# Kernel tuning notes

Hardware: AMD Instinct MI355X
Metric: run time of the kernel (lower is better)

The kernel has to match this reference:

```python
import jax, jax.numpy as jnp
import numpy as np

D_MODEL = 512
D_EMB = 300
D_FIXED = 30000
D_EXT = 32000
BS, L, J, N, T = 8, 256, 48, 32, 48


def setup_inputs() -> dict:
    key = jax.random.key(0)
    ks = jax.random.split(key, 32)
    s = 0.02
    def nrm(k, shape, scale=0.02):
        return jax.random.normal(k, shape, dtype=jnp.float32) * scale
    inp = {
        "Mp": jax.random.normal(ks[0], (BS, L, D_MODEL), dtype=jnp.float32),
        "Mq": jax.random.normal(ks[1], (BS, J, D_MODEL), dtype=jnp.float32),
        "Mqa": jax.random.normal(ks[2], (BS, N, D_MODEL), dtype=jnp.float32),
        "Mnlg": jax.random.normal(ks[3], (BS, T, D_MODEL), dtype=jnp.float32),
        "mask_p": jnp.ones((BS, L, 1), dtype=bool),
        "mask_q": jnp.ones((BS, J, 1), dtype=bool),
        "mask_qa": jnp.ones((BS, N, 1), dtype=bool),
        "source_ext": jax.random.randint(ks[4], (BS, L + J + N), 0, D_EXT, dtype=jnp.int64) if jax.config.jax_enable_x64 else jax.random.randint(ks[4], (BS, L + J + N), 0, D_EXT).astype(jnp.int32),
        "special_mask": jnp.ones((D_FIXED,), dtype=bool).at[jnp.array([0, 1, 2, 3])].set(False),
        "d_ext_vocab": D_EXT,
    }
    # additive attention params for question / qa / passage branches
    names = ["q", "a", "p"]
    for i, nme in enumerate(names):
        base = 5 + 5 * i
        inp[f"Wk_{nme}"] = nrm(ks[base + 0], (D_MODEL, D_MODEL))
        inp[f"bk_{nme}"] = jnp.zeros((D_MODEL,), dtype=jnp.float32)
        inp[f"Wq_{nme}"] = nrm(ks[base + 1], (D_MODEL, D_MODEL))
        inp[f"bq_{nme}"] = jnp.zeros((D_MODEL,), dtype=jnp.float32)
        inp[f"v_{nme}"] = nrm(ks[base + 2], (D_MODEL,))
    # vocab generator: Linear(d_model, d_emb) -> Linear(d_emb, d_fixed, bias=False)
    inp["W1"] = nrm(ks[20], (D_MODEL, D_EMB))
    inp["b1"] = jnp.zeros((D_EMB,), dtype=jnp.float32)
    inp["W2"] = nrm(ks[21], (D_EMB, D_FIXED))
    # mixture: Linear(4*d_model, 4) + softmax
    inp["Wm"] = nrm(ks[22], (4 * D_MODEL, 4))
    inp["bm"] = jnp.zeros((4,), dtype=jnp.float32)
    return inp


def _additive_attn(K, V, Q, mask, Wk, bk, Wq, bq, v):
    # K,V: [b,S,d]; Q: [b,T,d]; mask: [b,S,1] bool
    Kp = K @ Wk + bk                                  # [b,S,d]
    Qp = Q @ Wq + bq                                  # [b,T,d]
    scores = jnp.einsum("btsd,d->bts", jnp.tanh(Qp[:, :, None, :] + Kp[:, None, :, :]), v)
    scores = jnp.where(mask[:, None, :, 0], scores, -1e9)
    attn = jax.nn.softmax(scores, axis=-1)            # [b,T,S]
    ctx = jnp.einsum("bts,bsd->btd", attn, V)         # [b,T,d]
    return ctx, attn


def reference(Mp, Mq, Mqa, Mnlg, mask_p, mask_q, mask_qa, source_ext, special_mask,
              Wk_q, bk_q, Wq_q, bq_q, v_q,
              Wk_a, bk_a, Wq_a, bq_a, v_a,
              Wk_p, bk_p, Wq_p, bq_p, v_p,
              W1, b1, W2, Wm, bm, d_ext_vocab):
    d_fixed = special_mask.shape[0]
    bs, Tq, _ = Mnlg.shape

    ctx_q, q_distr = _additive_attn(Mq, Mq, Mnlg, mask_q, Wk_q, bk_q, Wq_q, bq_q, v_q)
    ctx_a, qa_distr = _additive_attn(Mqa, Mqa, Mnlg, mask_qa, Wk_a, bk_a, Wq_a, bq_a, v_a)
    ctx_p, p_distr = _additive_attn(Mp, Mp, Mnlg, mask_p, Wk_p, bk_p, Wq_p, bq_p, v_p)

    # fixed-vocab distribution with special tokens masked out
    logits = (Mnlg @ W1 + b1) @ W2                    # [b,T,d_fixed]
    logits = jnp.where(special_mask[None, None, :], logits, -1e9)
    fixed_vocab_distr = jax.nn.softmax(logits, axis=-1)

    # mixture weights
    mix_in = jnp.concatenate([Mnlg, ctx_q, ctx_a, ctx_p], axis=-1)  # [b,T,4d]
    lambdas = jax.nn.softmax(mix_in @ Wm + bm, axis=-1)             # [b,T,4]
    lam_v, lam_q, lam_qa, lam_p = jnp.split(lambdas, 4, axis=-1)

    fixed_vocab_distr = fixed_vocab_distr * lam_v
    source_distr = jnp.concatenate([p_distr * lam_p, q_distr * lam_q, qa_distr * lam_qa], axis=-1)  # [b,T,S_tot]

    # scatter-add over extended vocab (math-equivalent to one_hot + matmul)
    def _scatter(src, idx):
        # src: [T,S_tot], idx: [S_tot]
        return jnp.zeros((Tq, d_ext_vocab), src.dtype).at[:, idx].add(src)

    ext_vocab_distr = jax.vmap(_scatter)(source_distr, source_ext)  # [b,T,d_ext]
    ext_vocab_distr = ext_vocab_distr.at[:, :, :d_fixed].add(fixed_vocab_distr)
    return ext_vocab_distr, lambdas
```

## Files before the change

kernel.cpp:

```cpp
#include <hip/hip_runtime.h>
#include <math.h>

#define BS     8
#define LL     256
#define JJ     48
#define NN     32
#define TT     48
#define DM     512
#define DEMB   300
#define DFIX   30000
#define DEXT   32000
#define SRC_TOT (LL + JJ + NN)
#define ROWS   (BS * TT)
#define NT     235
#define KH     320

typedef float f32x4  __attribute__((ext_vector_type(4)));
typedef short bf16x8 __attribute__((ext_vector_type(8)));

__device__ __forceinline__ short f2bf(float f) {
    union { float f; unsigned u; } v; v.f = f;
    return (short)((v.u + 0x7FFFu + ((v.u >> 16) & 1u)) >> 16);
}
__device__ __forceinline__ float bf2f(short s) {
    union { unsigned u; float f; } v;
    v.u = ((unsigned)(unsigned short)s) << 16;
    return v.f;
}
__device__ __forceinline__ float fast_exp2(float x) {
#if __has_builtin(__builtin_amdgcn_exp2f)
    return __builtin_amdgcn_exp2f(x);
#else
    return exp2f(x);
#endif
}
__device__ __forceinline__ float fast_rcp(float x) {
#if __has_builtin(__builtin_amdgcn_rcpf)
    return __builtin_amdgcn_rcpf(x);
#else
    return 1.f / x;
#endif
}
__device__ __forceinline__ float fast_tanh(float x) {
    x = fminf(fmaxf(x, -15.f), 15.f);
    const float e = fast_exp2(x * 2.885390082f);
    return (e - 1.f) * fast_rcp(e + 1.f);
}
__device__ __forceinline__ bool smask_true(const void* smask, bool byteLayout, int i)
{
    if (byteLayout) return ((const unsigned char*)smask)[i] != 0;
    return ((const int*)smask)[i] != 0;
}
__device__ __forceinline__ void mask8(const void* smask, bool byteLayout, int i,
                                      int* mb)
{
    if (byteLayout) {
        const uchar4 a = ((const uchar4*)((const unsigned char*)smask + i))[0];
        const uchar4 b = ((const uchar4*)((const unsigned char*)smask + i))[1];
        mb[0]=a.x; mb[1]=a.y; mb[2]=a.z; mb[3]=a.w;
        mb[4]=b.x; mb[5]=b.y; mb[6]=b.z; mb[7]=b.w;
    } else {
        const int* p = (const int*)smask + i;
        #pragma unroll
        for (int j = 0; j < 8; ++j) mb[j] = p[j];
    }
}

struct PDesc { const float* src; short* dst; int K, N, Kp, ntx, tiles; };
struct PArgs { PDesc d[12]; int nd; };

__global__ __launch_bounds__(256) void prep_kernel(PArgs pa)
{
    __shared__ short T[64][72];
    int tile = blockIdx.x, g = 0;
    while (g + 1 < pa.nd && tile >= pa.d[g].tiles) { tile -= pa.d[g].tiles; ++g; }
    const PDesc d = pa.d[g];
    const int tid = threadIdx.x;

    if (d.ntx == 0) {
        const int i = (tile * 256 + tid) * 8;
        if (i < d.K) {
            const float4 a = ((const float4*)(d.src + i))[0];
            const float4 b = ((const float4*)(d.src + i))[1];
            bf16x8 v;
            v[0]=f2bf(a.x); v[1]=f2bf(a.y); v[2]=f2bf(a.z); v[3]=f2bf(a.w);
            v[4]=f2bf(b.x); v[5]=f2bf(b.y); v[6]=f2bf(b.z); v[7]=f2bf(b.w);
            *(bf16x8*)&d.dst[i] = v;
        }
        return;
    }
    const int kt = tile / d.ntx, nt = tile % d.ntx;
    const int k0 = kt * 64, n0 = nt * 64;
    {
        const int n = n0 + (tid & 63);
        #pragma unroll
        for (int p = 0; p < 16; ++p) {
            const int kk = p * 4 + (tid >> 6);
            const int k = k0 + kk;
            float v = 0.f;
            if (k < d.K && n < d.N) v = d.src[(size_t)k * d.N + n];
            T[kk][tid & 63] = f2bf(v);
        }
    }
    __syncthreads();
    {
        const int nn = tid >> 2;
        const int kq = (tid & 3) * 16;
        const int n = n0 + nn;
        if (n < d.N) {
            bf16x8 v0, v1;
            #pragma unroll
            for (int j = 0; j < 8; ++j) v0[j] = T[kq + j][nn];
            #pragma unroll
            for (int j = 0; j < 8; ++j) v1[j] = T[kq + 8 + j][nn];
            *(bf16x8*)&d.dst[(size_t)n * d.Kp + k0 + kq]     = v0;
            *(bf16x8*)&d.dst[(size_t)n * d.Kp + k0 + kq + 8] = v1;
        }
    }
}

struct GDesc { const short* A; const short* Bt; const float* bias; void* C;
               const void* smask; float* pstat;
               int M, N, K, Kp, nx, my, obf, npad, nt, tiles; };
struct GArgs { GDesc d[7]; int nd; };

__global__ __launch_bounds__(256) void gemm_bf16_kernel(GArgs ga)
{
    __shared__ short As[2][4][130][8];
    __shared__ short Bs[2][4][130][8];
    __shared__ float pm_s[128][2];
    __shared__ float ps_s[128][2];

    int tile = blockIdx.x, g = 0;
    while (g + 1 < ga.nd && tile >= ga.d[g].tiles) { tile -= ga.d[g].tiles; ++g; }
    const GDesc d = ga.d[g];
    const short* __restrict__ A  = d.A;
    const short* __restrict__ Bt = d.Bt;
    const float* bias = d.bias;
    const int N = d.N, Kp = d.Kp;
    const int nx = d.nx, my = d.my, obf = d.obf, npad = d.npad;

    int bm, bn;
    if (my > 0) { bm = (tile % my) * 128; bn = (tile / my) * 128; }
    else        { bm = (tile / nx) * 128; bn = (tile % nx) * 128; }
    const int tid  = threadIdx.x;
    const int lane = tid & 63;
    const int wv   = tid >> 6;
    const int wm   = (wv >> 1) * 64;
    const int wn   = (wv & 1) * 64;

    bf16x8 ra[2], rb[2];

    auto loadA = [&](int k0) {
        #pragma unroll
        for (int p = 0; p < 2; ++p) {
            const int row = p * 64 + (tid >> 2);
            ra[p] = *(const bf16x8*)&A[(size_t)(bm + row) * Kp + k0 + (tid & 3) * 8];
        }
    };
    auto loadB = [&](int k0) {
        #pragma unroll
        for (int p = 0; p < 2; ++p) {
            const int idx = p * 256 + tid;
            const int n = idx >> 2, kb = idx & 3;
            const int gn = bn + n;
            bf16x8 v = {};
            if (gn < N) v = *(const bf16x8*)&Bt[(size_t)gn * Kp + k0 + kb * 8];
            rb[p] = v;
        }
    };
    auto storeA = [&](int buf) {
        const int kb = tid & 3;
        #pragma unroll
        for (int p = 0; p < 2; ++p)
            *(bf16x8*)&As[buf][kb][p * 64 + (tid >> 2)][0] = ra[p];
    };
    auto storeB = [&](int buf) {
        #pragma unroll
        for (int p = 0; p < 2; ++p) {
            const int idx = p * 256 + tid;
            const int n = idx >> 2, kb = idx & 3;
            *(bf16x8*)&Bs[buf][kb][n][0] = rb[p];
        }
    };

    f32x4 acc[4][4] = {};
    const int nk = Kp / 32;

    loadA(0); loadB(0);
    storeA(0); storeB(0);
    __syncthreads();

    for (int kk = 0; kk < nk; ++kk) {
        const int cur = kk & 1;
        if (kk + 1 < nk) { loadA((kk + 1) * 32); loadB((kk + 1) * 32); }
        bf16x8 af[4], bfr[4];
        #pragma unroll
        for (int i = 0; i < 4; ++i) {
            af[i]  = *(const bf16x8*)&As[cur][lane >> 4][wm + i * 16 + (lane & 15)][0];
            bfr[i] = *(const bf16x8*)&Bs[cur][lane >> 4][wn + i * 16 + (lane & 15)][0];
        }
        #pragma unroll
        for (int mi = 0; mi < 4; ++mi)
            #pragma unroll
            for (int ni = 0; ni < 4; ++ni)
                acc[mi][ni] = __builtin_amdgcn_mfma_f32_16x16x32_bf16(
                    af[mi], bfr[ni], acc[mi][ni], 0, 0, 0);
        if (kk + 1 < nk) { storeA(cur ^ 1); storeB(cur ^ 1); }
        __syncthreads();
    }

    if (obf == 0) {
        float* Cf = (float*)d.C;
        #pragma unroll
        for (int ni = 0; ni < 4; ++ni) {
            const int gn = bn + wn + ni * 16 + (lane & 15);
            if (gn >= N) continue;
            const float bb = bias ? bias[gn] : 0.f;
            #pragma unroll
            for (int mi = 0; mi < 4; ++mi)
                #pragma unroll
                for (int r = 0; r < 4; ++r) {
                    const int gm = bm + wm + mi * 16 + (lane >> 4) * 4 + r;
                    Cf[(size_t)gm * N + gn] = acc[mi][ni][r] + bb;
                }
        }
    } else if (obf == 2) {
        short* Cs = (short*)d.C;
        #pragma unroll
        for (int ni = 0; ni < 4; ++ni) {
            const int gn = bn + wn + ni * 16 + (lane & 15);
            if (gn >= npad) continue;
            const bool valid = (gn < N);
            const float bb = (valid && bias) ? bias[gn] : 0.f;
            #pragma unroll
            for (int mi = 0; mi < 4; ++mi)
                #pragma unroll
                for (int r = 0; r < 4; ++r) {
                    const int gm = bm + wm + mi * 16 + (lane >> 4) * 4 + r;
                    Cs[(size_t)gm * npad + gn] = valid ? f2bf(acc[mi][ni][r] + bb) : (short)0;
                }
        }
    } else {
        short* Cs = (short*)d.C;
        const void* sm2 = d.smask;
        const bool byteLayout = (((const int*)sm2)[1] == 0x01010101);
        int mk[4];
        #pragma unroll
        for (int ni = 0; ni < 4; ++ni) {
            const int gn = bn + wn + ni * 16 + (lane & 15);
            const bool inb = (gn < N);
            mk[ni] = inb && smask_true(sm2, byteLayout, inb ? gn : 0);
            if (inb) {
                #pragma unroll
                for (int mi = 0; mi < 4; ++mi)
                    #pragma unroll
                    for (int r = 0; r < 4; ++r) {
                        const int gm = bm + wm + mi * 16 + (lane >> 4) * 4 + r;
                        Cs[(size_t)gm * N + gn] = f2bf(acc[mi][ni][r]);
                    }
            }
        }
        #pragma unroll
        for (int mi = 0; mi < 4; ++mi) {
            #pragma unroll
            for (int r = 0; r < 4; ++r) {
                const int rl = wm + mi * 16 + (lane >> 4) * 4 + r;
                float vmax = -INFINITY;
                #pragma unroll
                for (int ni = 0; ni < 4; ++ni)
                    if (mk[ni]) vmax = fmaxf(vmax, acc[mi][ni][r]);
                #pragma unroll
                for (int o = 1; o < 16; o <<= 1)
                    vmax = fmaxf(vmax, __shfl_xor(vmax, o));
                float se = 0.f;
                #pragma unroll
                for (int ni = 0; ni < 4; ++ni)
                    if (mk[ni]) se += __expf(acc[mi][ni][r] - vmax);
                #pragma unroll
                for (int o = 1; o < 16; o <<= 1)
                    se += __shfl_xor(se, o);
                if ((lane & 15) == 0) {
                    pm_s[rl][wn >> 6] = vmax;
                    ps_s[rl][wn >> 6] = se;
                }
            }
        }
        __syncthreads();
        if (tid < 128) {
            const float mA = pm_s[tid][0], mB = pm_s[tid][1];
            const float sA = ps_s[tid][0], sB = ps_s[tid][1];
            const float m = fmaxf(mA, mB);
            float s = 0.f;
            if (sA > 0.f) s += sA * __expf(mA - m);
            if (sB > 0.f) s += sB * __expf(mB - m);
            float* ps = d.pstat;
            const size_t idx = ((size_t)(bm + tid) * d.nt + (bn >> 7)) * 2;
            ps[idx + 0] = m;
            ps[idx + 1] = s;
        }
    }
}

struct SDesc { const short* Kp; const short* Qp; const float* vv;
               int Sb, s0, cnt, off; };
struct SArgs { SDesc c[6]; };

__global__ __launch_bounds__(256) void scores_kernel(SArgs sa,
                                                     float* __restrict__ scb)
{
    const SDesc d = sa.c[blockIdx.y];
    const int bt   = blockIdx.x;
    const int b    = bt / TT;
    const int tid  = threadIdx.x;
    const int lane = tid & 63;
    const int wave = tid >> 6;

    float qp[8], vv[8];
    {
        const bf16x8 q = *(const bf16x8*)&d.Qp[(size_t)bt * DM + lane * 8];
        #pragma unroll
        for (int j = 0; j < 8; ++j) qp[j] = bf2f(q[j]);
        const float4 a = ((const float4*)(d.vv + lane * 8))[0];
        const float4 c = ((const float4*)(d.vv + lane * 8))[1];
        vv[0]=a.x; vv[1]=a.y; vv[2]=a.z; vv[3]=a.w;
        vv[4]=c.x; vv[5]=c.y; vv[6]=c.z; vv[7]=c.w;
    }
    for (int s = wave; s < d.cnt; s += 4) {
        const bf16x8 kv = *(const bf16x8*)&d.Kp[((size_t)b * d.Sb + d.s0 + s) * DM + lane * 8];
        float acc = 0.f;
        #pragma unroll
        for (int j = 0; j < 8; ++j)
            acc = fmaf(vv[j], fast_tanh(qp[j] + bf2f(kv[j])), acc);
        #pragma unroll
        for (int off = 32; off; off >>= 1) acc += __shfl_xor(acc, off);
        if (lane == 0) scb[(size_t)bt * SRC_TOT + d.off + s] = acc;
    }
}

__global__ __launch_bounds__(512) void attn2mix_kernel(
    const float* __restrict__ scb,
    const short* __restrict__ Mqb, const short* __restrict__ Mqab,
    const short* __restrict__ Mpb, const float* __restrict__ Mnlg,
    const float* __restrict__ Wm, const float* __restrict__ bm,
    const float* __restrict__ pstat,
    float* __restrict__ vals, float* __restrict__ stat,
    float* __restrict__ lam_out)
{
    __shared__ float a_sh[SRC_TOT];
    __shared__ float part[4][DM];
    __shared__ float cQ[DM], cA[DM], cP[DM];
    __shared__ float red[16];
    __shared__ float redm[32];
    __shared__ float s_lam[4];
    const int bt   = blockIdx.x;
    const int b    = bt / TT;
    const int tid  = threadIdx.x;
    const int lane = tid & 63;
    const int wave = tid >> 6;
    const float* srow = scb + (size_t)bt * SRC_TOT;

    #pragma unroll
    for (int br = 0; br < 3; ++br) {
        const int off = (br == 0) ? 0 : (br == 1) ? JJ : (JJ + NN);
        const int cnt = (br == 0) ? JJ : (br == 1) ? NN : LL;
        float x = (tid < cnt) ? srow[off + tid] : -INFINITY;
        float m = x;
        #pragma unroll
        for (int o = 32; o; o >>= 1) m = fmaxf(m, __shfl_xor(m, o));
        if (lane == 0) red[wave] = m;
        __syncthreads();
        m = red[0];
        #pragma unroll
        for (int w = 1; w < 8; ++w) m = fmaxf(m, red[w]);
        float e = (tid < cnt) ? __expf(x - m) : 0.f;
        float ss = e;
        #pragma unroll
        for (int o = 32; o; o >>= 1) ss += __shfl_xor(ss, o);
        if (lane == 0) red[8 + wave] = ss;
        __syncthreads();
        float denom = 0.f;
        #pragma unroll
        for (int w = 0; w < 8; ++w) denom += red[8 + w];
        if (tid < cnt) a_sh[off + tid] = e / denom;
        __syncthreads();
    }
    {
        const int sq = tid >> 7;
        const int dq = (tid & 127) * 4;
        float p0 = 0.f, p1 = 0.f, p2 = 0.f, p3 = 0.f;
        for (int s = sq; s < JJ; s += 4) {
            const float a = a_sh[s];
            const short4 v = *(const short4*)&Mqb[((size_t)b * JJ + s) * DM + dq];
            p0 = fmaf(a, bf2f(v.x), p0); p1 = fmaf(a, bf2f(v.y), p1);
            p2 = fmaf(a, bf2f(v.z), p2); p3 = fmaf(a, bf2f(v.w), p3);
        }
        part[sq][dq+0]=p0; part[sq][dq+1]=p1; part[sq][dq+2]=p2; part[sq][dq+3]=p3;
        __syncthreads();
        cQ[tid] = part[0][tid] + part[1][tid] + part[2][tid] + part[3][tid];
        __syncthreads();
        p0 = p1 = p2 = p3 = 0.f;
        for (int s = sq; s < NN; s += 4) {
            const float a = a_sh[JJ + s];
            const short4 v = *(const short4*)&Mqab[((size_t)b * NN + s) * DM + dq];
            p0 = fmaf(a, bf2f(v.x), p0); p1 = fmaf(a, bf2f(v.y), p1);
            p2 = fmaf(a, bf2f(v.z), p2); p3 = fmaf(a, bf2f(v.w), p3);
        }
        part[sq][dq+0]=p0; part[sq][dq+1]=p1; part[sq][dq+2]=p2; part[sq][dq+3]=p3;
        __syncthreads();
        cA[tid] = part[0][tid] + part[1][tid] + part[2][tid] + part[3][tid];
        __syncthreads();
        p0 = p1 = p2 = p3 = 0.f;
        for (int s = sq; s < LL; s += 4) {
            const float a = a_sh[JJ + NN + s];
            const short4 v = *(const short4*)&Mpb[((size_t)b * LL + s) * DM + dq];
            p0 = fmaf(a, bf2f(v.x), p0); p1 = fmaf(a, bf2f(v.y), p1);
            p2 = fmaf(a, bf2f(v.z), p2); p3 = fmaf(a, bf2f(v.w), p3);
        }
        part[sq][dq+0]=p0; part[sq][dq+1]=p1; part[sq][dq+2]=p2; part[sq][dq+3]=p3;
        __syncthreads();
        cP[tid] = part[0][tid] + part[1][tid] + part[2][tid] + part[3][tid];
        __syncthreads();
    }
    {
        const float x0 = Mnlg[(size_t)bt * DM + tid];
        const float x1 = cQ[tid], x2 = cA[tid], x3 = cP[tid];
        const float4 w0 = *(const float4*)&Wm[(size_t)tid * 4];
        const float4 w1 = *(const float4*)&Wm[(size_t)(512 + tid) * 4];
        const float4 w2 = *(const float4*)&Wm[(size_t)(1024 + tid) * 4];
        const float4 w3 = *(const float4*)&Wm[(size_t)(1536 + tid) * 4];
        float acc[4];
        acc[0] = x0 * w0.x + x1 * w1.x + x2 * w2.x + x3 * w3.x;
        acc[1] = x0 * w0.y + x1 * w1.y + x2 * w2.y + x3 * w3.y;
        acc[2] = x0 * w0.z + x1 * w1.z + x2 * w2.z + x3 * w3.z;
        acc[3] = x0 * w0.w + x1 * w1.w + x2 * w2.w + x3 * w3.w;
        #pragma unroll
        for (int c = 0; c < 4; ++c)
            #pragma unroll
            for (int o = 32; o; o >>= 1) acc[c] += __shfl_xor(acc[c], o);
        if (lane == 0) {
            redm[wave * 4 + 0] = acc[0]; redm[wave * 4 + 1] = acc[1];
            redm[wave * 4 + 2] = acc[2]; redm[wave * 4 + 3] = acc[3];
        }
        __syncthreads();
        if (tid == 0) {
            float l[4];
            #pragma unroll
            for (int c = 0; c < 4; ++c) {
                float s = bm[c];
                #pragma unroll
                for (int w = 0; w < 8; ++w) s += redm[w * 4 + c];
                l[c] = s;
            }
            const float mx = fmaxf(fmaxf(l[0], l[1]), fmaxf(l[2], l[3]));
            const float e0 = __expf(l[0] - mx), e1 = __expf(l[1] - mx);
            const float e2 = __expf(l[2] - mx), e3 = __expf(l[3] - mx);
            const float inv = 1.f / (e0 + e1 + e2 + e3);
            s_lam[0] = e0 * inv; s_lam[1] = e1 * inv;
            s_lam[2] = e2 * inv; s_lam[3] = e3 * inv;
            lam_out[bt * 4 + 0] = e0 * inv; lam_out[bt * 4 + 1] = e1 * inv;
            lam_out[bt * 4 + 2] = e2 * inv; lam_out[bt * 4 + 3] = e3 * inv;
        }
    }
    __syncthreads();
    if (wave == 0) {
        float m = -INFINITY;
        for (int c = lane; c < NT; c += 64)
            m = fmaxf(m, pstat[((size_t)bt * NT + c) * 2]);
        #pragma unroll
        for (int o = 32; o; o >>= 1) m = fmaxf(m, __shfl_xor(m, o));
        float s = 0.f;
        for (int c = lane; c < NT; c += 64) {
            const float pm = pstat[((size_t)bt * NT + c) * 2];
            const float ps = pstat[((size_t)bt * NT + c) * 2 + 1];
            if (ps > 0.f) s += ps * __expf(pm - m);
        }
        #pragma unroll
        for (int o = 32; o; o >>= 1) s += __shfl_xor(s, o);
        if (lane == 0) {
            stat[bt * 2 + 0] = m;
            stat[bt * 2 + 1] = s_lam[0] / s;
        }
    }
    if (tid < SRC_TOT) {
        float val;
        if      (tid < LL)      val = a_sh[JJ + NN + tid]        * s_lam[3];
        else if (tid < LL + JJ) val = a_sh[tid - LL]             * s_lam[1];
        else                    val = a_sh[JJ + (tid - LL - JJ)] * s_lam[2];
        vals[(size_t)bt * SRC_TOT + tid] = val;
    }
}

__global__ __launch_bounds__(256) void writescatter_kernel(
    const short* __restrict__ logits, const void* __restrict__ smask,
    const float* __restrict__ stat, const float* __restrict__ vals,
    const void* __restrict__ src_ext, float* __restrict__ out)
{
    const bool byteLayout = (((const int*)smask)[1] == 0x01010101);
    const int r  = blockIdx.x;
    const int c0 = blockIdx.y * 4096;
    const float m   = stat[r * 2 + 0];
    const float inv = stat[r * 2 + 1];
    const short* lrow = logits + (size_t)r * DFIX;
    float* orow = out + (size_t)r * DEXT;
    const int tid = threadIdx.x;

    #pragma unroll
    for (int k = 0; k < 2; ++k) {
        const int i = c0 + (k * 256 + tid) * 8;
        if (i >= DEXT) continue;
        float4 o0 = make_float4(0.f, 0.f, 0.f, 0.f);
        float4 o1 = make_float4(0.f, 0.f, 0.f, 0.f);
        if (i < DFIX) {
            const bf16x8 v = *(const bf16x8*)&lrow[i];
            int mb[8]; mask8(smask, byteLayout, i, mb);
            o0.x = mb[0] ? __expf(bf2f(v[0]) - m) * inv : 0.f;
            o0.y = mb[1] ? __expf(bf2f(v[1]) - m) * inv : 0.f;
            o0.z = mb[2] ? __expf(bf2f(v[2]) - m) * inv : 0.f;
            o0.w = mb[3] ? __expf(bf2f(v[3]) - m) * inv : 0.f;
            o1.x = mb[4] ? __expf(bf2f(v[4]) - m) * inv : 0.f;
            o1.y = mb[5] ? __expf(bf2f(v[5]) - m) * inv : 0.f;
            o1.z = mb[6] ? __expf(bf2f(v[6]) - m) * inv : 0.f;
            o1.w = mb[7] ? __expf(bf2f(v[7]) - m) * inv : 0.f;
        }
        *(float4*)&orow[i]     = o0;
        *(float4*)&orow[i + 4] = o1;
    }
    __syncthreads();
    {
        const int* s32 = (const int*)src_ext;
        const bool src64 = (s32[1] == 0 && s32[3] == 0 && s32[5] == 0 && s32[7] == 0);
        const int b = r / TT;
        for (int p = tid; p < SRC_TOT; p += 256) {
            const int pos = b * SRC_TOT + p;
            const int idx = src64 ? (int)((const long long*)src_ext)[pos] : s32[pos];
            if (idx >= c0 && idx < c0 + 4096)
                atomicAdd(&orow[idx], vals[(size_t)r * SRC_TOT + p]);
        }
    }
}

extern "C" void kernel_launch(void* const* d_in, const int* in_sizes, int n_in,
                              void* d_out, int out_size, void* d_ws, size_t ws_size,
                              hipStream_t stream)
{
    const float* Mp   = (const float*)d_in[0];
    const float* Mq   = (const float*)d_in[1];
    const float* Mqa  = (const float*)d_in[2];
    const float* Mnlg = (const float*)d_in[3];
    const void* src_ext = d_in[7];
    const void* smask   = d_in[8];
    const float* Wk_q = (const float*)d_in[10];
    const float* bk_q = (const float*)d_in[11];
    const float* Wq_q = (const float*)d_in[12];
    const float* bq_q = (const float*)d_in[13];
    const float* v_q  = (const float*)d_in[14];
    const float* Wk_a = (const float*)d_in[15];
    const float* bk_a = (const float*)d_in[16];
    const float* Wq_a = (const float*)d_in[17];
    const float* bq_a = (const float*)d_in[18];
    const float* v_a  = (const float*)d_in[19];
    const float* Wk_p = (const float*)d_in[20];
    const float* bk_p = (const float*)d_in[21];
    const float* Wq_p = (const float*)d_in[22];
    const float* bq_p = (const float*)d_in[23];
    const float* v_p  = (const float*)d_in[24];
    const float* W1   = (const float*)d_in[25];
    const float* b1   = (const float*)d_in[26];
    const float* W2   = (const float*)d_in[27];
    const float* Wm   = (const float*)d_in[28];
    const float* bm   = (const float*)d_in[29];
    float* out = (float*)d_out;

    char* ws = (char*)d_ws;
    size_t off = 0;
    auto alloc = [&](size_t bytes) -> char* {
        char* p = ws + off;
        off += (bytes + 255) & ~(size_t)255;
        return p;
    };
    short* logits = (short*)alloc((size_t)ROWS * DFIX * 2);
    short* KpP    = (short*)alloc((size_t)BS * LL * DM * 2);
    short* KpQ    = (short*)alloc((size_t)BS * JJ * DM * 2);
    short* KpA    = (short*)alloc((size_t)BS * NN * DM * 2);
    short* QpQ    = (short*)alloc((size_t)ROWS * DM * 2);
    short* QpA    = (short*)alloc((size_t)ROWS * DM * 2);
    short* QpP    = (short*)alloc((size_t)ROWS * DM * 2);
    float* pstat  = (float*)alloc((size_t)ROWS * NT * 2 * 4);
    float* scb    = (float*)alloc((size_t)ROWS * SRC_TOT * 4);
    float* vals   = (float*)alloc((size_t)ROWS * SRC_TOT * 4);
    float* stat   = (float*)alloc((size_t)ROWS * 2 * 4);
    short* tWkq = (short*)alloc((size_t)DM * DM * 2);
    short* tWqq = (short*)alloc((size_t)DM * DM * 2);
    short* tWka = (short*)alloc((size_t)DM * DM * 2);
    short* tWqa = (short*)alloc((size_t)DM * DM * 2);
    short* tWkp = (short*)alloc((size_t)DM * DM * 2);
    short* tWqp = (short*)alloc((size_t)DM * DM * 2);
    short* tW1  = (short*)alloc((size_t)DEMB * DM * 2);
    short* tW2  = (short*)alloc((size_t)DFIX * KH * 2);
    short* Mp_bf   = (short*)alloc((size_t)BS * LL * DM * 2);
    short* Mq_bf   = (short*)alloc((size_t)BS * JJ * DM * 2);
    short* Mqa_bf  = (short*)alloc((size_t)BS * NN * DM * 2);
    short* Mnlg_bf = (short*)alloc((size_t)ROWS * DM * 2);
    short* Hh_bf   = (short*)alloc((size_t)ROWS * KH * 2);
    (void)ws_size; (void)in_sizes; (void)n_in; (void)out_size;

    PArgs p1;
    p1.nd = 12;
    p1.d[0]  = { Wk_p, tWkp, DM,   DM,   DM, 8, 64 };
    p1.d[1]  = { Wk_q, tWkq, DM,   DM,   DM, 8, 64 };
    p1.d[2]  = { Wk_a, tWka, DM,   DM,   DM, 8, 64 };
    p1.d[3]  = { Wq_q, tWqq, DM,   DM,   DM, 8, 64 };
    p1.d[4]  = { Wq_a, tWqa, DM,   DM,   DM, 8, 64 };
    p1.d[5]  = { Wq_p, tWqp, DM,   DM,   DM, 8, 64 };
    p1.d[6]  = { W1,   tW1,  DM,   DEMB, DM, 5, 40 };
    p1.d[7]  = { W2,   tW2,  DEMB, DFIX, KH, 469, 2345 };
    p1.d[8]  = { Mp,   Mp_bf,   BS*LL*DM, 0, 0, 0, (BS*LL*DM) / 2048 };
    p1.d[9]  = { Mq,   Mq_bf,   BS*JJ*DM, 0, 0, 0, (BS*JJ*DM) / 2048 };
    p1.d[10] = { Mqa,  Mqa_bf,  BS*NN*DM, 0, 0, 0, (BS*NN*DM) / 2048 };
    p1.d[11] = { Mnlg, Mnlg_bf, ROWS*DM,  0, 0, 0, (ROWS*DM) / 2048 };
    prep_kernel<<<64 * 6 + 40 + 2345 + 512 + 96 + 64 + 96, 256, 0, stream>>>(p1);

    GArgs g2;
    g2.nd = 1;
    g2.d[0] = { Mnlg_bf, tW1, b1, Hh_bf, nullptr, nullptr,
                ROWS, DEMB, DM, DM, 3, 0, 2, KH, 0, 9 };
    gemm_bf16_kernel<<<9, 256, 0, stream>>>(g2);

    GArgs g3;
    g3.nd = 7;
    g3.d[0] = { Mp_bf,   tWkp, bk_p, KpP, nullptr, nullptr,
                BS*LL, DM, DM, DM, 4, 0, 2, DM, 0, 64 };
    g3.d[1] = { Mq_bf,   tWkq, bk_q, KpQ, nullptr, nullptr,
                BS*JJ, DM, DM, DM, 4, 0, 2, DM, 0, 12 };
    g3.d[2] = { Mqa_bf,  tWka, bk_a, KpA, nullptr, nullptr,
                BS*NN, DM, DM, DM, 4, 0, 2, DM, 0, 8 };
    g3.d[3] = { Mnlg_bf, tWqq, bq_q, QpQ, nullptr, nullptr,
                ROWS, DM, DM, DM, 4, 0, 2, DM, 0, 12 };
    g3.d[4] = { Mnlg_bf, tWqa, bq_a, QpA, nullptr, nullptr,
                ROWS, DM, DM, DM, 4, 0, 2, DM, 0, 12 };
    g3.d[5] = { Mnlg_bf, tWqp, bq_p, QpP, nullptr, nullptr,
                ROWS, DM, DM, DM, 4, 0, 2, DM, 0, 12 };
    g3.d[6] = { Hh_bf,   tW2,  nullptr, logits, smask, pstat,
                ROWS, DFIX, DEMB, KH, 235, 3, 1, DFIX, NT, 705 };
    gemm_bf16_kernel<<<825, 256, 0, stream>>>(g3);

    SArgs sa;
    sa.c[0] = { KpQ, QpQ, v_q, JJ,   0, JJ,  0 };
    sa.c[1] = { KpA, QpA, v_a, NN,   0, NN,  JJ };
    sa.c[2] = { KpP, QpP, v_p, LL,   0, 64,  JJ + NN };
    sa.c[3] = { KpP, QpP, v_p, LL,  64, 64,  JJ + NN + 64 };
    sa.c[4] = { KpP, QpP, v_p, LL, 128, 64,  JJ + NN + 128 };
    sa.c[5] = { KpP, QpP, v_p, LL, 192, 64,  JJ + NN + 192 };
    scores_kernel<<<dim3(ROWS, 6), 256, 0, stream>>>(sa, scb);

    attn2mix_kernel<<<ROWS, 512, 0, stream>>>(
        scb, Mq_bf, Mqa_bf, Mp_bf, Mnlg, Wm, bm, pstat,
        vals, stat, out + (size_t)ROWS * DEXT);

    writescatter_kernel<<<dim3(ROWS, 8), 256, 0, stream>>>(
        logits, smask, stat, vals, src_ext, out);
}
```

Before: 152.9 us.

## Precompute mixture projections of memories so attn2mix avoids context vectors

Uses linearity: ctx @ Wm_slice equals attention weights times (M @ Wm_slice). The prep kernel now projects every Mq, Mqa and Mp row onto the 4 mixture outputs, and Mnlg onto its slice plus bias. attn2mix then takes a 336-term weighted sum of 4-vectors per row instead of reading whole bf16 memory matrices to build three 512-dim contexts. This removes a large per-row memory read and several barriers, at the cost of extra prep blocks. It also uses fp32 inputs rather than bf16, which slightly changes numerics.

```diff
diff --git a/kernel.cpp b/kernel.cpp
--- a/kernel.cpp
+++ b/kernel.cpp
@@ -67,7 +67,7 @@
 }
 
 struct PDesc { const float* src; short* dst; int K, N, Kp, ntx, tiles; };
-struct PArgs { PDesc d[12]; int nd; };
+struct PArgs { PDesc d[16]; int nd; const float* Wm; const float* bm; };
 
 __global__ __launch_bounds__(256) void prep_kernel(PArgs pa)
 {
@@ -76,6 +76,44 @@
     while (g + 1 < pa.nd && tile >= pa.d[g].tiles) { tile -= pa.d[g].tiles; ++g; }
     const PDesc d = pa.d[g];
     const int tid = threadIdx.x;
+
+    if (d.ntx == -1) {
+        const int r = tile * 4 + (tid >> 6);
+        const int lane = tid & 63;
+        if (r >= d.K) return;
+        const int s0 = d.Kp;
+        const int woff = (s0 < 0) ? 0 : (s0 == 0) ? 512 : (s0 == 48) ? 1024 : 1536;
+        const float4* xp = (const float4*)(d.src + (size_t)r * DM) + lane * 2;
+        const float4 x0 = xp[0], x1 = xp[1];
+        const float xv[8] = { x0.x, x0.y, x0.z, x0.w, x1.x, x1.y, x1.z, x1.w };
+        const float4* wp = (const float4*)(pa.Wm + (size_t)(woff + lane * 8) * 4);
+        float acc[4] = {0.f, 0.f, 0.f, 0.f};
+        #pragma unroll
+        for (int j = 0; j < 8; ++j) {
+            const float4 w = wp[j];
+            acc[0] = fmaf(xv[j], w.x, acc[0]);
+            acc[1] = fmaf(xv[j], w.y, acc[1]);
+            acc[2] = fmaf(xv[j], w.z, acc[2]);
+            acc[3] = fmaf(xv[j], w.w, acc[3]);
+        }
+        #pragma unroll
+        for (int c = 0; c < 4; ++c)
+            #pragma unroll
+            for (int o = 32; o; o >>= 1) acc[c] += __shfl_xor(acc[c], o);
+        if (lane == 0) {
+            float* dst = (float*)d.dst;
+            if (s0 < 0) {
+                #pragma unroll
+                for (int c = 0; c < 4; ++c) dst[r * 4 + c] = acc[c] + pa.bm[c];
+            } else {
+                const int b = r / d.N, s = r % d.N;
+                #pragma unroll
+                for (int c = 0; c < 4; ++c)
+                    dst[((size_t)b * SRC_TOT + s0 + s) * 4 + c] = acc[c];
+            }
+        }
+        return;
+    }
 
     if (d.ntx == 0) {
         const int i = (tile * 256 + tid) * 8;
@@ -340,16 +378,13 @@
 
 __global__ __launch_bounds__(512) void attn2mix_kernel(
     const float* __restrict__ scb,
-    const short* __restrict__ Mqb, const short* __restrict__ Mqab,
-    const short* __restrict__ Mpb, const float* __restrict__ Mnlg,
-    const float* __restrict__ Wm, const float* __restrict__ bm,
+    const float* __restrict__ Vall,
+    const float* __restrict__ base,
     const float* __restrict__ pstat,
     float* __restrict__ vals, float* __restrict__ stat,
     float* __restrict__ lam_out)
 {
     __shared__ float a_sh[SRC_TOT];
-    __shared__ float part[4][DM];
-    __shared__ float cQ[DM], cA[DM], cP[DM];
     __shared__ float red[16];
     __shared__ float redm[32];
     __shared__ float s_lam[4];
@@ -386,68 +421,27 @@
         __syncthreads();
     }
     {
-        const int sq = tid >> 7;
-        const int dq = (tid & 127) * 4;
-        float p0 = 0.f, p1 = 0.f, p2 = 0.f, p3 = 0.f;
-        for (int s = sq; s < JJ; s += 4) {
-            const float a = a_sh[s];
-            const short4 v = *(const short4*)&Mqb[((size_t)b * JJ + s) * DM + dq];
-            p0 = fmaf(a, bf2f(v.x), p0); p1 = fmaf(a, bf2f(v.y), p1);
-            p2 = fmaf(a, bf2f(v.z), p2); p3 = fmaf(a, bf2f(v.w), p3);
-        }
-        part[sq][dq+0]=p0; part[sq][dq+1]=p1; part[sq][dq+2]=p2; part[sq][dq+3]=p3;
-        __syncthreads();
-        cQ[tid] = part[0][tid] + part[1][tid] + part[2][tid] + part[3][tid];
-        __syncthreads();
-        p0 = p1 = p2 = p3 = 0.f;
-        for (int s = sq; s < NN; s += 4) {
-            const float a = a_sh[JJ + s];
-            const short4 v = *(const short4*)&Mqab[((size_t)b * NN + s) * DM + dq];
-            p0 = fmaf(a, bf2f(v.x), p0); p1 = fmaf(a, bf2f(v.y), p1);
-            p2 = fmaf(a, bf2f(v.z), p2); p3 = fmaf(a, bf2f(v.w), p3);
-        }
-        part[sq][dq+0]=p0; part[sq][dq+1]=p1; part[sq][dq+2]=p2; part[sq][dq+3]=p3;
-        __syncthreads();
-        cA[tid] = part[0][tid] + part[1][tid] + part[2][tid] + part[3][tid];
-        __syncthreads();
-        p0 = p1 = p2 = p3 = 0.f;
-        for (int s = sq; s < LL; s += 4) {
-            const float a = a_sh[JJ + NN + s];
-            const short4 v = *(const short4*)&Mpb[((size_t)b * LL + s) * DM + dq];
-            p0 = fmaf(a, bf2f(v.x), p0); p1 = fmaf(a, bf2f(v.y), p1);
-            p2 = fmaf(a, bf2f(v.z), p2); p3 = fmaf(a, bf2f(v.w), p3);
-        }
-        part[sq][dq+0]=p0; part[sq][dq+1]=p1; part[sq][dq+2]=p2; part[sq][dq+3]=p3;
-        __syncthreads();
-        cP[tid] = part[0][tid] + part[1][tid] + part[2][tid] + part[3][tid];
-        __syncthreads();
-    }
-    {
-        const float x0 = Mnlg[(size_t)bt * DM + tid];
-        const float x1 = cQ[tid], x2 = cA[tid], x3 = cP[tid];
-        const float4 w0 = *(const float4*)&Wm[(size_t)tid * 4];
-        const float4 w1 = *(const float4*)&Wm[(size_t)(512 + tid) * 4];
-        const float4 w2 = *(const float4*)&Wm[(size_t)(1024 + tid) * 4];
-        const float4 w3 = *(const float4*)&Wm[(size_t)(1536 + tid) * 4];
-        float acc[4];
-        acc[0] = x0 * w0.x + x1 * w1.x + x2 * w2.x + x3 * w3.x;
-        acc[1] = x0 * w0.y + x1 * w1.y + x2 * w2.y + x3 * w3.y;
-        acc[2] = x0 * w0.z + x1 * w1.z + x2 * w2.z + x3 * w3.z;
-        acc[3] = x0 * w0.w + x1 * w1.w + x2 * w2.w + x3 * w3.w;
-        #pragma unroll
-        for (int c = 0; c < 4; ++c)
-            #pragma unroll
-            for (int o = 32; o; o >>= 1) acc[c] += __shfl_xor(acc[c], o);
+        float c0 = 0.f, c1 = 0.f, c2 = 0.f, c3 = 0.f;
+        if (tid < SRC_TOT) {
+            const float a = a_sh[tid];
+            const float4 v = *(const float4*)&Vall[((size_t)b * SRC_TOT + tid) * 4];
+            c0 = a * v.x; c1 = a * v.y; c2 = a * v.z; c3 = a * v.w;
+        }
+        #pragma unroll
+        for (int o = 32; o; o >>= 1) {
+            c0 += __shfl_xor(c0, o); c1 += __shfl_xor(c1, o);
+            c2 += __shfl_xor(c2, o); c3 += __shfl_xor(c3, o);
+        }
         if (lane == 0) {
-            redm[wave * 4 + 0] = acc[0]; redm[wave * 4 + 1] = acc[1];
-            redm[wave * 4 + 2] = acc[2]; redm[wave * 4 + 3] = acc[3];
+            redm[wave * 4 + 0] = c0; redm[wave * 4 + 1] = c1;
+            redm[wave * 4 + 2] = c2; redm[wave * 4 + 3] = c3;
         }
         __syncthreads();
         if (tid == 0) {
             float l[4];
             #pragma unroll
             for (int c = 0; c < 4; ++c) {
-                float s = bm[c];
+                float s = base[bt * 4 + c];
                 #pragma unroll
                 for (int w = 0; w < 8; ++w) s += redm[w * 4 + c];
                 l[c] = s;
@@ -590,6 +584,8 @@
     float* scb    = (float*)alloc((size_t)ROWS * SRC_TOT * 4);
     float* vals   = (float*)alloc((size_t)ROWS * SRC_TOT * 4);
     float* stat   = (float*)alloc((size_t)ROWS * 2 * 4);
+    float* Vall   = (float*)alloc((size_t)BS * SRC_TOT * 4 * 4);
+    float* baseV  = (float*)alloc((size_t)ROWS * 4 * 4);
     short* tWkq = (short*)alloc((size_t)DM * DM * 2);
     short* tWqq = (short*)alloc((size_t)DM * DM * 2);
     short* tWka = (short*)alloc((size_t)DM * DM * 2);
@@ -606,7 +602,8 @@
     (void)ws_size; (void)in_sizes; (void)n_in; (void)out_size;
 
     PArgs p1;
-    p1.nd = 12;
+    p1.nd = 16;
+    p1.Wm = Wm; p1.bm = bm;
     p1.d[0]  = { Wk_p, tWkp, DM,   DM,   DM, 8, 64 };
     p1.d[1]  = { Wk_q, tWkq, DM,   DM,   DM, 8, 64 };
     p1.d[2]  = { Wk_a, tWka, DM,   DM,   DM, 8, 64 };
@@ -619,7 +616,12 @@
     p1.d[9]  = { Mq,   Mq_bf,   BS*JJ*DM, 0, 0, 0, (BS*JJ*DM) / 2048 };
     p1.d[10] = { Mqa,  Mqa_bf,  BS*NN*DM, 0, 0, 0, (BS*NN*DM) / 2048 };
     p1.d[11] = { Mnlg, Mnlg_bf, ROWS*DM,  0, 0, 0, (ROWS*DM) / 2048 };
-    prep_kernel<<<64 * 6 + 40 + 2345 + 512 + 96 + 64 + 96, 256, 0, stream>>>(p1);
+    p1.d[12] = { Mnlg, (short*)baseV, ROWS,  0,  -1, -1,  96 };
+    p1.d[13] = { Mq,   (short*)Vall,  BS*JJ, JJ,  0, -1,  96 };
+    p1.d[14] = { Mqa,  (short*)Vall,  BS*NN, NN, 48, -1,  64 };
+    p1.d[15] = { Mp,   (short*)Vall,  BS*LL, LL, 80, -1, 512 };
+    prep_kernel<<<64*6 + 40 + 2345 + 512 + 96 + 64 + 96 + 96 + 96 + 64 + 512,
+                  256, 0, stream>>>(p1);
 
     GArgs g2;
     g2.nd = 1;
@@ -655,8 +657,7 @@
     scores_kernel<<<dim3(ROWS, 6), 256, 0, stream>>>(sa, scb);
 
     attn2mix_kernel<<<ROWS, 512, 0, stream>>>(
-        scb, Mq_bf, Mqa_bf, Mp_bf, Mnlg, Wm, bm, pstat,
-        vals, stat, out + (size_t)ROWS * DEXT);
+        scb, Vall, baseV, pstat, vals, stat, out + (size_t)ROWS * DEXT);
 
     writescatter_kernel<<<dim3(ROWS, 8), 256, 0, stream>>>(
         logits, smask, stat, vals, src_ext, out);
```

New measurement: 134.0 us. -12.3%, faster.
